# Optimization experiments

Measured on AMD Instinct MI355X. Metric: run time of the kernel, lower is better.

Reference implementation:

```python
import jax, jax.numpy as jnp
import numpy as np

G, N, C_IN, C_OUT, HEADS = 64, 2048, 64, 64, 2
E = 1_000_000
T = G * N  # total flattened nodes
NEG_SLOPE = 0.2  # PyG GATv2Conv default


def setup_inputs() -> dict:
    key = jax.random.key(0)
    k_x, k_e, k_wl, k_wr, k_a, k_b = jax.random.split(key, 6)
    x = jax.random.normal(k_x, (G, N, C_IN), dtype=jnp.float32)
    edge_index = jax.random.randint(k_e, (2, E), 0, T, dtype=jnp.int64)
    # GATv2Conv params (share_weights=False): separate lin_l / lin_r, per-head att vector, bias
    s = 1.0 / np.sqrt(C_IN)
    W_l = jax.random.uniform(k_wl, (C_IN, HEADS * C_OUT), minval=-s, maxval=s, dtype=jnp.float32)
    W_r = jax.random.uniform(k_wr, (C_IN, HEADS * C_OUT), minval=-s, maxval=s, dtype=jnp.float32)
    att = jax.random.normal(k_a, (HEADS, C_OUT), dtype=jnp.float32) * 0.1
    bias = jax.random.normal(k_b, (HEADS * C_OUT,), dtype=jnp.float32) * 0.01
    return {"x": x, "edge_index": edge_index, "W_l": W_l, "W_r": W_r, "att": att, "bias": bias}


def reference(x, edge_index, W_l, W_r, att, bias):
    # Flatten batched nodes: (G, N, C_in) -> (T, C_in)
    x_flat = x.reshape(-1, C_IN)
    # Linear projections per side, split heads: (T, H, C)
    xl = (x_flat @ W_l).reshape(T, HEADS, C_OUT)
    xr = (x_flat @ W_r).reshape(T, HEADS, C_OUT)
    # add_self_loops=True: append (i, i) for every flattened node
    loop = jnp.arange(T, dtype=edge_index.dtype)
    src = jnp.concatenate([edge_index[0], loop])
    dst = jnp.concatenate([edge_index[1], loop])
    # GATv2 scoring: e_ij = att . LeakyReLU(xl[j] + xr[i])  -> (E', H)
    h = jax.nn.leaky_relu(xl[src] + xr[dst], negative_slope=NEG_SLOPE)
    score = jnp.einsum('ehc,hc->eh', h, att)
    # Segment softmax over incoming edges of each destination node
    m = jax.ops.segment_max(score, dst, num_segments=T)  # (T, H)
    ealpha = jnp.exp(score - m[dst])
    denom = jax.ops.segment_sum(ealpha, dst, num_segments=T)
    alpha = ealpha / denom[dst]  # self-loops guarantee denom > 0
    # Scatter-aggregate messages: out[i] = sum_j alpha_ij * xl[j]
    out = jax.ops.segment_sum(alpha[:, :, None] * xl[src], dst, num_segments=T)  # (T, H, C)
    out = out.reshape(T, HEADS * C_OUT) + bias
    return out.reshape(G, N, HEADS * C_OUT)
```

## Files before the change

### kernel.cpp

```cpp
#include <hip/hip_runtime.h>
#include <hip/hip_bf16.h>

#define T_NODES (64 * 2048)
#define CIN 64
#define HC 128
#define NEG_SLOPE 0.2f
#define GEMM_BLOCKS (T_NODES / 64)

typedef unsigned short ushort_t;
typedef __attribute__((ext_vector_type(8))) short bf16x8;
typedef __attribute__((ext_vector_type(4))) float f32x4;

__device__ __forceinline__ ushort_t f2bf(float x) {
    unsigned u = __float_as_uint(x);
    u += 0x7fffu + ((u >> 16) & 1u);
    return (ushort_t)(u >> 16);
}
__device__ __forceinline__ float bf2f(ushort_t b) {
    return __uint_as_float(((unsigned)b) << 16);
}

__global__ void prep_w(const float* __restrict__ Wl, const float* __restrict__ Wr,
                       uint4* __restrict__ wt) {
    const int t = blockIdx.x * 256 + threadIdx.x;
    const int n = t & 255, cc = t >> 8;
    const float* Wsrc = ((n < HC) ? Wl : Wr) + (n & (HC - 1));
    union { ushort_t u[8]; uint4 v; } pk;
#pragma unroll
    for (int j = 0; j < 8; ++j) pk.u[j] = f2bf(Wsrc[(cc * 8 + j) * HC]);
    const int sw = (n & 7) << 4;
    *(uint4*)((char*)wt + n * 128 + ((cc * 16) ^ sw)) = pk.v;
}

__global__ __launch_bounds__(256) void gemm_hist(const float* __restrict__ x,
                                                 const uint4* __restrict__ wt,
                                                 ushort_t* __restrict__ xl,
                                                 ushort_t* __restrict__ xr,
                                                 const int* __restrict__ ei,
                                                 unsigned* __restrict__ counts,
                                                 ushort_t* __restrict__ rank,
                                                 int E, int ET, int histBlocks) {
    __shared__ uint4 lds4[2560];
    const int tid = threadIdx.x;

    if (blockIdx.x < histBlocks) {
        const int b = blockIdx.x;
#pragma unroll
        for (int e = 0; e < 4; ++e) {
            int i = b * 1024 + e * 256 + tid;
            if (i < ET) {
                int dst = (i < E) ? ei[E + i] : (i - E);
                rank[i] = (ushort_t)atomicAdd(&counts[dst], 1u);
            }
        }
        return;
    }

    char* abase = (char*)lds4;
    char* wbase = (char*)lds4 + 8192;
    const int row0 = (blockIdx.x - histBlocks) * 64;

    {
        const int r = tid >> 2, c4 = tid & 3;
        const float4* xp = (const float4*)(x + (size_t)(row0 + r) * CIN + c4 * 16);
        float4 f0 = xp[0], f1 = xp[1], f2 = xp[2], f3 = xp[3];
        union { ushort_t u[16]; uint4 v[2]; } pk;
        const float s[16] = {f0.x,f0.y,f0.z,f0.w, f1.x,f1.y,f1.z,f1.w,
                             f2.x,f2.y,f2.z,f2.w, f3.x,f3.y,f3.z,f3.w};
#pragma unroll
        for (int j = 0; j < 16; ++j) pk.u[j] = f2bf(s[j]);
        const int sw = (r & 7) << 4;
        *(uint4*)(abase + r * 128 + ((c4 * 32)      ^ sw)) = pk.v[0];
        *(uint4*)(abase + r * 128 + ((c4 * 32 + 16) ^ sw)) = pk.v[1];
    }
    {
#pragma unroll
        for (int q = 0; q < 8; ++q)
            lds4[512 + q * 256 + tid] = wt[q * 256 + tid];
    }
    __syncthreads();

    const int wave = tid >> 6;
    const int lane = tid & 63;
    const int ar = lane & 15;
    const int kb = lane >> 4;

    bf16x8 afr[2][4], bfr[2][4];
#pragma unroll
    for (int kk = 0; kk < 2; ++kk) {
#pragma unroll
        for (int rt = 0; rt < 4; ++rt) {
            const int r = rt * 16 + ar;
            afr[kk][rt] = *(bf16x8*)(abase + r * 128 + ((kk * 64 + kb * 16) ^ ((r & 7) << 4)));
        }
#pragma unroll
        for (int ct = 0; ct < 4; ++ct) {
            const int n = wave * 64 + ct * 16 + ar;
            bfr[kk][ct] = *(bf16x8*)(wbase + n * 128 + ((kk * 64 + kb * 16) ^ ((n & 7) << 4)));
        }
    }

    f32x4 acc[4][4];
#pragma unroll
    for (int rt = 0; rt < 4; ++rt)
#pragma unroll
        for (int ct = 0; ct < 4; ++ct) acc[rt][ct] = (f32x4){0.f, 0.f, 0.f, 0.f};

#pragma unroll
    for (int kk = 0; kk < 2; ++kk)
#pragma unroll
        for (int rt = 0; rt < 4; ++rt)
#pragma unroll
            for (int ct = 0; ct < 4; ++ct)
                acc[rt][ct] = __builtin_amdgcn_mfma_f32_16x16x32_bf16(
                    afr[kk][rt], bfr[kk][ct], acc[rt][ct], 0, 0, 0);

    ushort_t* op = (wave < 2) ? xl : xr;
    const int colbase = (wave & 1) * 64 + ar;
    const int rowoff = (lane >> 4) * 4;
#pragma unroll
    for (int rt = 0; rt < 4; ++rt)
#pragma unroll
        for (int ct = 0; ct < 4; ++ct)
#pragma unroll
            for (int j = 0; j < 4; ++j)
                op[(size_t)(row0 + rt * 16 + rowoff + j) * HC + colbase + ct * 16] =
                    f2bf(acc[rt][ct][j]);
}

__global__ __launch_bounds__(256) void scan_tiles(const unsigned* __restrict__ counts,
                                                  unsigned* __restrict__ offs,
                                                  unsigned* __restrict__ partials) {
    __shared__ unsigned s[256];
    const int t = threadIdx.x;
    const int base = blockIdx.x * 1024 + t * 4;
    uint4 c = *(const uint4*)(counts + base);
    unsigned mysum = c.x + c.y + c.z + c.w;
    s[t] = mysum;
    __syncthreads();
    for (int off = 1; off < 256; off <<= 1) {
        unsigned v = (t >= off) ? s[t - off] : 0u;
        __syncthreads();
        s[t] += v;
        __syncthreads();
    }
    unsigned excl = s[t] - mysum;
    uint4 o;
    o.x = excl;
    o.y = excl + c.x;
    o.z = o.y + c.y;
    o.w = o.z + c.z;
    *(uint4*)(offs + base) = o;
    if (t == 255) partials[blockIdx.x] = s[255];
}

__global__ __launch_bounds__(256) void finalize_offs(unsigned* __restrict__ offs,
                                                     const unsigned* __restrict__ partials) {
    __shared__ unsigned s[128];
    const int t = threadIdx.x;
    const int tile = blockIdx.x >> 2;
    if (t < 128) s[t] = (t < tile) ? partials[t] : 0u;
    __syncthreads();
    for (int off = 64; off; off >>= 1) {
        if (t < off) s[t] += s[t + off];
        __syncthreads();
    }
    const unsigned base = s[0];
    const int i = blockIdx.x * 256 + t;
    offs[i] += base;
}

__global__ void scatter_edges(const int* __restrict__ ei,
                              const unsigned* __restrict__ offs,
                              const ushort_t* __restrict__ rank,
                              int* __restrict__ sorted_src, int E, int ET) {
    int i = blockIdx.x * 256 + threadIdx.x;
    if (i >= ET) return;
    int src, dst;
    if (i < E) { src = ei[i]; dst = ei[E + i]; }
    else       { src = dst = i - E; }
    sorted_src[offs[dst] + rank[i]] = src;
}

__global__ __launch_bounds__(256) void fused_aggr(const ushort_t* __restrict__ xl,
                                                  const ushort_t* __restrict__ xr,
                                                  const int* __restrict__ sorted_src,
                                                  const unsigned* __restrict__ offs,
                                                  const unsigned* __restrict__ counts,
                                                  const float* __restrict__ att,
                                                  const float* __restrict__ bias,
                                                  float* __restrict__ out) {
    const int lane = threadIdx.x & 63;
    int node = (blockIdx.x * 256 + threadIdx.x) >> 6;
    node = __builtin_amdgcn_readfirstlane(node);

    const float2 att2 = ((const float2*)att)[lane];
    const ushort2 xrv = ((const ushort2*)xr)[(size_t)node * 64 + lane];
    const float xr0 = bf2f(xrv.x), xr1 = bf2f(xrv.y);

    const int start = (int)offs[node];
    const int cnt   = (int)counts[node];
    const ushort2* xl2 = (const ushort2*)xl;

    float d = 0.f, acc0 = 0.f, acc1 = 0.f;

#define SCORE(a0, a1, p)                                                    \
    {                                                                       \
        float h0 = (a0) + xr0; h0 = h0 > 0.f ? h0 : NEG_SLOPE * h0;         \
        float h1 = (a1) + xr1; h1 = h1 > 0.f ? h1 : NEG_SLOPE * h1;         \
        p = att2.x * h0 + att2.y * h1;                                      \
    }
#define MERGE(p, a0, a1)                                                    \
    {                                                                       \
        float e = __expf(p);                                                \
        d += e;                                                             \
        acc0 += e * (a0);                                                   \
        acc1 += e * (a1);                                                   \
    }

    int k = 0;
    for (; k + 4 <= cnt; k += 4) {
        const int s0 = sorted_src[start + k];
        const int s1 = sorted_src[start + k + 1];
        const int s2 = sorted_src[start + k + 2];
        const int s3 = sorted_src[start + k + 3];
        const ushort2 v0 = xl2[(size_t)s0 * 64 + lane];
        const ushort2 v1 = xl2[(size_t)s1 * 64 + lane];
        const ushort2 v2 = xl2[(size_t)s2 * 64 + lane];
        const ushort2 v3 = xl2[(size_t)s3 * 64 + lane];
        const float a00 = bf2f(v0.x), a01 = bf2f(v0.y);
        const float a10 = bf2f(v1.x), a11 = bf2f(v1.y);
        const float a20 = bf2f(v2.x), a21 = bf2f(v2.y);
        const float a30 = bf2f(v3.x), a31 = bf2f(v3.y);
        float p0, p1, p2, p3;
        SCORE(a00, a01, p0);
        SCORE(a10, a11, p1);
        SCORE(a20, a21, p2);
        SCORE(a30, a31, p3);
#pragma unroll
        for (int off = 16; off; off >>= 1) {
            p0 += __shfl_xor(p0, off);
            p1 += __shfl_xor(p1, off);
            p2 += __shfl_xor(p2, off);
            p3 += __shfl_xor(p3, off);
        }
        MERGE(p0, a00, a01);
        MERGE(p1, a10, a11);
        MERGE(p2, a20, a21);
        MERGE(p3, a30, a31);
    }
    for (; k < cnt; ++k) {
        const int s0 = sorted_src[start + k];
        const ushort2 v0 = xl2[(size_t)s0 * 64 + lane];
        const float a00 = bf2f(v0.x), a01 = bf2f(v0.y);
        float p0;
        SCORE(a00, a01, p0);
#pragma unroll
        for (int off = 16; off; off >>= 1) p0 += __shfl_xor(p0, off);
        MERGE(p0, a00, a01);
    }

    const float2 b2 = ((const float2*)bias)[lane];
    float2 o;
    o.x = acc0 / d + b2.x;
    o.y = acc1 / d + b2.y;
    ((float2*)out)[(size_t)node * 64 + lane] = o;
}

extern "C" void kernel_launch(void* const* d_in, const int* in_sizes, int n_in,
                              void* d_out, int out_size, void* d_ws, size_t ws_size,
                              hipStream_t stream) {
    const float* x    = (const float*)d_in[0];
    const int*   ei   = (const int*)d_in[1];
    const float* Wl   = (const float*)d_in[2];
    const float* Wr   = (const float*)d_in[3];
    const float* att  = (const float*)d_in[4];
    const float* bias = (const float*)d_in[5];
    float* out = (float*)d_out;

    const int E  = in_sizes[1] / 2;
    const int ET = E + T_NODES;

    ushort_t* xl = (ushort_t*)d_ws;
    ushort_t* xr = xl + (size_t)T_NODES * HC;
    int* sorted_src = (int*)(xr + (size_t)T_NODES * HC);
    unsigned* counts   = (unsigned*)(sorted_src + ET);
    unsigned* offs     = counts + T_NODES;
    unsigned* partials = offs + T_NODES;
    ushort_t* rank     = (ushort_t*)(partials + 128);
    uint4* wt          = (uint4*)(rank + ((ET + 7) & ~7));

    hipMemsetAsync(counts, 0, (size_t)T_NODES * sizeof(unsigned), stream);

    prep_w<<<8, 256, 0, stream>>>(Wl, Wr, wt);

    const int histBlocks = (ET + 1023) / 1024;
    gemm_hist<<<histBlocks + GEMM_BLOCKS, 256, 0, stream>>>(x, wt, xl, xr,
                                                            ei, counts, rank,
                                                            E, ET, histBlocks);

    scan_tiles<<<T_NODES / 1024, 256, 0, stream>>>(counts, offs, partials);
    finalize_offs<<<T_NODES / 256, 256, 0, stream>>>(offs, partials);
    int eblocks = (ET + 255) / 256;
    scatter_edges<<<eblocks, 256, 0, stream>>>(ei, offs, rank, sorted_src, E, ET);

    fused_aggr<<<T_NODES / 4, 256, 0, stream>>>(xl, xr, sorted_src, offs, counts,
                                                att, bias, out);
}
```

Measured before the change: 164.0 us.

## Split wavefront into four edge slots with 16-byte per-lane gathers

The aggregation kernel now assigns each wavefront's 64 lanes to four edge slots of 16 lanes each, so one wavefront processes four incoming edges at once. Each lane loads 8 bf16 features with a single 16-byte load instead of 2 features per lane. Per-edge score reduction drops to three shuffles within 8-lane groups, and the partial sums across slots are combined once at the end of the node. This cuts shuffle and instruction overhead per edge and widens memory transactions, at the cost of more registers and idle lanes when a node's degree is not a multiple of four.

New measurement: 163.7 us. Within noise of the previous version (-0.2%).

```diff
diff --git a/kernel.cpp b/kernel.cpp
--- a/kernel.cpp
+++ b/kernel.cpp
@@ -190,81 +190,79 @@
                                                   const float* __restrict__ att,
                                                   const float* __restrict__ bias,
                                                   float* __restrict__ out) {
-    const int lane = threadIdx.x & 63;
-    int node = (blockIdx.x * 256 + threadIdx.x) >> 6;
+    const int tid = threadIdx.x;
+    const int lane = tid & 63;
+    int node = (blockIdx.x * 256 + tid) >> 6;
     node = __builtin_amdgcn_readfirstlane(node);
-
-    const float2 att2 = ((const float2*)att)[lane];
-    const ushort2 xrv = ((const ushort2*)xr)[(size_t)node * 64 + lane];
-    const float xr0 = bf2f(xrv.x), xr1 = bf2f(xrv.y);
+    const int slot = lane >> 4;
+    const int sub  = lane & 15;
+    const int cb   = sub * 8;
+
+    float attv[8], xrv[8];
+    {
+        const float4 a0 = *(const float4*)(att + cb);
+        const float4 a1 = *(const float4*)(att + cb + 4);
+        attv[0]=a0.x; attv[1]=a0.y; attv[2]=a0.z; attv[3]=a0.w;
+        attv[4]=a1.x; attv[5]=a1.y; attv[6]=a1.z; attv[7]=a1.w;
+        const uint4 xv = *(const uint4*)(xr + (size_t)node * HC + cb);
+        const ushort_t* xu = (const ushort_t*)&xv;
+#pragma unroll
+        for (int j = 0; j < 8; ++j) xrv[j] = bf2f(xu[j]);
+    }
 
     const int start = (int)offs[node];
     const int cnt   = (int)counts[node];
-    const ushort2* xl2 = (const ushort2*)xl;
-
-    float d = 0.f, acc0 = 0.f, acc1 = 0.f;
-
-#define SCORE(a0, a1, p)                                                    \
-    {                                                                       \
-        float h0 = (a0) + xr0; h0 = h0 > 0.f ? h0 : NEG_SLOPE * h0;         \
-        float h1 = (a1) + xr1; h1 = h1 > 0.f ? h1 : NEG_SLOPE * h1;         \
-        p = att2.x * h0 + att2.y * h1;                                      \
-    }
-#define MERGE(p, a0, a1)                                                    \
-    {                                                                       \
-        float e = __expf(p);                                                \
-        d += e;                                                             \
-        acc0 += e * (a0);                                                   \
-        acc1 += e * (a1);                                                   \
-    }
-
-    int k = 0;
-    for (; k + 4 <= cnt; k += 4) {
-        const int s0 = sorted_src[start + k];
-        const int s1 = sorted_src[start + k + 1];
-        const int s2 = sorted_src[start + k + 2];
-        const int s3 = sorted_src[start + k + 3];
-        const ushort2 v0 = xl2[(size_t)s0 * 64 + lane];
-        const ushort2 v1 = xl2[(size_t)s1 * 64 + lane];
-        const ushort2 v2 = xl2[(size_t)s2 * 64 + lane];
-        const ushort2 v3 = xl2[(size_t)s3 * 64 + lane];
-        const float a00 = bf2f(v0.x), a01 = bf2f(v0.y);
-        const float a10 = bf2f(v1.x), a11 = bf2f(v1.y);
-        const float a20 = bf2f(v2.x), a21 = bf2f(v2.y);
-        const float a30 = bf2f(v3.x), a31 = bf2f(v3.y);
-        float p0, p1, p2, p3;
-        SCORE(a00, a01, p0);
-        SCORE(a10, a11, p1);
-        SCORE(a20, a21, p2);
-        SCORE(a30, a31, p3);
-#pragma unroll
-        for (int off = 16; off; off >>= 1) {
-            p0 += __shfl_xor(p0, off);
-            p1 += __shfl_xor(p1, off);
-            p2 += __shfl_xor(p2, off);
-            p3 += __shfl_xor(p3, off);
+    const int rounds = (cnt + 3) >> 2;
+
+    float acc[8];
+#pragma unroll
+    for (int j = 0; j < 8; ++j) acc[j] = 0.f;
+    float d = 0.f;
+
+    for (int r = 0; r < rounds; ++r) {
+        const int k = r * 4 + slot;
+        const bool valid = k < cnt;
+        const int src = sorted_src[start + (valid ? k : 0)];
+        const uint4 v = *(const uint4*)(xl + (size_t)src * HC + cb);
+        const ushort_t* vu = (const ushort_t*)&v;
+        float a[8];
+        float p = 0.f;
+#pragma unroll
+        for (int j = 0; j < 8; ++j) {
+            a[j] = bf2f(vu[j]);
+            float z = a[j] + xrv[j];
+            float lr = z > 0.f ? z : NEG_SLOPE * z;
+            p = __builtin_fmaf(attv[j], lr, p);
         }
-        MERGE(p0, a00, a01);
-        MERGE(p1, a10, a11);
-        MERGE(p2, a20, a21);
-        MERGE(p3, a30, a31);
-    }
-    for (; k < cnt; ++k) {
-        const int s0 = sorted_src[start + k];
-        const ushort2 v0 = xl2[(size_t)s0 * 64 + lane];
-        const float a00 = bf2f(v0.x), a01 = bf2f(v0.y);
-        float p0;
-        SCORE(a00, a01, p0);
-#pragma unroll
-        for (int off = 16; off; off >>= 1) p0 += __shfl_xor(p0, off);
-        MERGE(p0, a00, a01);
-    }
-
-    const float2 b2 = ((const float2*)bias)[lane];
-    float2 o;
-    o.x = acc0 / d + b2.x;
-    o.y = acc1 / d + b2.y;
-    ((float2*)out)[(size_t)node * 64 + lane] = o;
+        p += __shfl_xor(p, 1);
+        p += __shfl_xor(p, 2);
+        p += __shfl_xor(p, 4);
+        const float e = valid ? __expf(p) : 0.f;
+        d += e;
+#pragma unroll
+        for (int j = 0; j < 8; ++j) acc[j] = __builtin_fmaf(e, a[j], acc[j]);
+    }
+
+#pragma unroll
+    for (int off = 16; off <= 32; off <<= 1) {
+        d += __shfl_xor(d, off);
+#pragma unroll
+        for (int j = 0; j < 8; ++j) acc[j] += __shfl_xor(acc[j], off);
+    }
+
+    if (slot == 0) {
+        const float inv = 1.f / d;
+        const float4 b0 = *(const float4*)(bias + cb);
+        const float4 b1 = *(const float4*)(bias + cb + 4);
+        float4 o0, o1;
+        o0.x = acc[0] * inv + b0.x; o0.y = acc[1] * inv + b0.y;
+        o0.z = acc[2] * inv + b0.z; o0.w = acc[3] * inv + b0.w;
+        o1.x = acc[4] * inv + b1.x; o1.y = acc[5] * inv + b1.y;
+        o1.z = acc[6] * inv + b1.z; o1.w = acc[7] * inv + b1.w;
+        float* op = out + (size_t)node * HC + cb;
+        *(float4*)op = o0;
+        *(float4*)(op + 4) = o1;
+    }
 }
 
 extern "C" void kernel_launch(void* const* d_in, const int* in_sizes, int n_in,
```
